# Optimization experiments

Measured on AMD Instinct MI355X. Metric: run time of the kernel, lower is better.

The kernel has to match this reference:

```python
import jax, jax.numpy as jnp
import numpy as np

B, H, W = 16, 1024, 1024
BOUNDARY_WEIGHT = 2.0
FOCAL_ALPHA = 0.25
FOCAL_GAMMA = 2.0
SMOOTH = 1e-6


def setup_inputs() -> dict:
    key = jax.random.key(0)
    k1, k2, k3 = jax.random.split(key, 3)
    pred_masks = jax.random.normal(k1, (B, 1, H, W), dtype=jnp.float32)
    gt_masks = jax.random.bernoulli(k2, 0.5, (B, 1, H, W)).astype(jnp.float32)
    pred_iou = jax.random.uniform(k3, (B, 1), dtype=jnp.float32)
    return {"pred_masks": pred_masks, "gt_masks": gt_masks, "pred_iou": pred_iou}


def _bce_with_logits(x, t):
    # stable: softplus(x) - x*t == -[t*log(sig(x)) + (1-t)*log(1-sig(x))]
    return jax.nn.softplus(x) - x * t


def reference(pred_masks, gt_masks, pred_iou):
    x, t = pred_masks, gt_masks
    ce = _bce_with_logits(x, t)                      # (B,1,H,W)
    p = jax.nn.sigmoid(x)

    # focal loss
    p_t = p * t + (1.0 - p) * (1.0 - t)
    alpha_t = FOCAL_ALPHA * t + (1.0 - FOCAL_ALPHA) * (1.0 - t)
    focal = jnp.mean(alpha_t * ce * (1.0 - p_t) ** FOCAL_GAMMA)

    # dice loss
    intersection = jnp.sum(p * t, axis=(2, 3))       # (B,1)
    union = jnp.sum(p, axis=(2, 3)) + jnp.sum(t, axis=(2, 3))
    dice = 1.0 - jnp.mean((2.0 * intersection + SMOOTH) / (union + SMOOTH))

    # boundary-weighted BCE. In the source, dist = EDT(mask) is 0 at every
    # background pixel and dist_inv = EDT(1-mask) is 0 at every foreground
    # pixel, so min(dist, dist_inv) == 0 <= 3 at EVERY pixel -> the weight
    # map is uniformly boundary_weight. Faithful equivalent:
    boundary = BOUNDARY_WEIGHT * jnp.mean(ce)

    total = focal + dice + 0.5 * boundary

    # IoU auxiliary loss (thresholded prediction; no grad flows through >0.5)
    pred_bin = (p > 0.5).astype(x.dtype)
    inter = jnp.sum(pred_bin * t, axis=(1, 2, 3))    # (B,)
    uni = jnp.sum(pred_bin, axis=(1, 2, 3)) + jnp.sum(t, axis=(1, 2, 3)) - inter
    actual_iou = (inter + SMOOTH) / (uni + SMOOTH)
    iou_loss = jnp.mean((jnp.squeeze(pred_iou) - actual_iou) ** 2)

    return total + 0.1 * iou_loss
```

## Files before the change

### kernel.cpp

```cpp
#include <hip/hip_runtime.h>
#include <math.h>


#define HW_PIX (1024 * 1024)
#define BATCH 16
constexpr int BPI = 256;
constexpr int GRID = BATCH * BPI;
constexpr int THREADS = 256;
constexpr int STRIDE_PX = BPI * THREADS * 4;
constexpr int ITERS = HW_PIX / STRIDE_PX;

__global__ __launch_bounds__(THREADS) void
loss_partial(const float* __restrict__ x, const float* __restrict__ t,
             float* __restrict__ acc) {
  const int b = blockIdx.x >> 8;
  const int chunk = blockIdx.x & (BPI - 1);
  const long base =
      (long)b * HW_PIX + ((long)chunk * THREADS + threadIdx.x) * 4;

  float fsum = 0.f, csum = 0.f, isum = 0.f, psum = 0.f;
  unsigned tcnt = 0, bicnt = 0, bpcnt = 0;

#pragma unroll
  for (int i = 0; i < ITERS; ++i) {
    const float4 xv = *(const float4*)(x + base + (long)i * STRIDE_PX);
    const float4 tv = *(const float4*)(t + base + (long)i * STRIDE_PX);
    const float* xs = reinterpret_cast<const float*>(&xv);
    const float* ts = reinterpret_cast<const float*>(&tv);
#pragma unroll
    for (int j = 0; j < 4; ++j) {
      const float xx = xs[j];
      const float tt = ts[j];
      const float e = __expf(-fabsf(xx));
      const float sp = 1.0f + e;
      const float r = __builtin_amdgcn_rcpf(sp);
      const float p = (xx >= 0.0f) ? r : e * r;
      const float ce = fmaxf(xx, 0.0f) - xx * tt + __logf(sp);
      const float om = fmaf(tt, 1.0f - 2.0f * p, p);
      const float at = 0.75f - 0.5f * tt;
      fsum += at * ce * om * om;
      csum += ce;
      isum = fmaf(p, tt, isum);
      psum += p;
      const unsigned long long mt = __ballot(tt != 0.0f);
      const unsigned long long mb = __ballot(xx > 0.0f);
      tcnt += (unsigned)__popcll(mt);
      bpcnt += (unsigned)__popcll(mb);
      bicnt += (unsigned)__popcll(mt & mb);
    }
  }

  __shared__ float red[THREADS / 64][7];
  const int lane = threadIdx.x & 63;
  const int wave = threadIdx.x >> 6;
  float vals[4] = {fsum, csum, isum, psum};
#pragma unroll
  for (int k = 0; k < 4; ++k) {
    float v = vals[k];
#pragma unroll
    for (int off = 32; off > 0; off >>= 1) v += __shfl_down(v, off);
    if (lane == 0) red[wave][k] = v;
  }
  if (lane == 0) {
    red[wave][4] = (float)tcnt;
    red[wave][5] = (float)bicnt;
    red[wave][6] = (float)bpcnt;
  }
  __syncthreads();
  if (threadIdx.x < 7) {
    acc[blockIdx.x * 7 + threadIdx.x] =
        red[0][threadIdx.x] + red[1][threadIdx.x] +
        red[2][threadIdx.x] + red[3][threadIdx.x];
  }
}

__global__ void loss_final(const float* __restrict__ acc,
                           const float* __restrict__ pred_iou,
                           float* __restrict__ out) {
  constexpr float SMOOTH = 1e-6f;
  __shared__ float fin[BATCH][7];
  const int tid = threadIdx.x;
  if (tid < BATCH * 7) {
    const int b = tid / 7, k = tid % 7;
    float s = 0.f;
    for (int i = 0; i < BPI; ++i)
      s += acc[(b * BPI + i) * 7 + k];
    fin[b][k] = s;
  }
  __syncthreads();
  if (tid < 64) {
    const int lane = tid;
    float F = 0.f, C = 0.f, D = 0.f, Q = 0.f;
    if (lane < BATCH) {
      F = fin[lane][0];
      C = fin[lane][1];
      const float I = fin[lane][2], P = fin[lane][3], T = fin[lane][4],
                  BI = fin[lane][5], BP = fin[lane][6];
      D = (2.0f * I + SMOOTH) / (P + T + SMOOTH);
      const float iou = (BI + SMOOTH) / (BP + T - BI + SMOOTH);
      const float d = pred_iou[lane] - iou;
      Q = d * d;
    }
#pragma unroll
    for (int off = 32; off > 0; off >>= 1) {
      F += __shfl_down(F, off);
      C += __shfl_down(C, off);
      D += __shfl_down(D, off);
      Q += __shfl_down(Q, off);
    }
    if (lane == 0) {
      const float invN = 1.0f / (float)((long)BATCH * HW_PIX);
      const float focal = F * invN;
      const float dice = 1.0f - D * (1.0f / (float)BATCH);
      const float half_boundary = C * invN;
      const float iou_loss = Q * (1.0f / (float)BATCH);
      out[0] = focal + dice + half_boundary + 0.1f * iou_loss;
    }
  }
}

extern "C" void kernel_launch(void* const* d_in, const int* in_sizes, int n_in,
                              void* d_out, int out_size, void* d_ws,
                              size_t ws_size, hipStream_t stream) {
  const float* x = (const float*)d_in[0];
  const float* t = (const float*)d_in[1];
  const float* piou = (const float*)d_in[2];
  float* acc = (float*)d_ws;

  loss_partial<<<GRID, THREADS, 0, stream>>>(x, t, acc);
  loss_final<<<1, 128, 0, stream>>>(acc, piou, (float*)d_out);
}
```

Before: 157.8 us.

## Issue all loads upfront via inline asm and consume with staged vmcnt waits

Halves the blocks per image so each thread handles eight float4 pairs. All sixteen global_load_dwordx4 instructions are issued up front through inline assembly using an SGPR base plus a VGPR offset. Each pair is then consumed after an explicit s_waitcnt vmcnt countdown. The intent is to keep many loads in flight per wave and to start compute as soon as the earliest data arrives, at the cost of more VGPRs and fewer blocks.

```diff
diff --git a/kernel.cpp b/kernel.cpp
--- a/kernel.cpp
+++ b/kernel.cpp
@@ -4,33 +4,42 @@
 
 #define HW_PIX (1024 * 1024)
 #define BATCH 16
-constexpr int BPI = 256;
+constexpr int BPI = 128;
 constexpr int GRID = BATCH * BPI;
 constexpr int THREADS = 256;
-constexpr int STRIDE_PX = BPI * THREADS * 4;
-constexpr int ITERS = HW_PIX / STRIDE_PX;
+constexpr unsigned SWEEP_B = BPI * THREADS * 16;
+
+typedef float vf4 __attribute__((ext_vector_type(4)));
 
 __global__ __launch_bounds__(THREADS) void
 loss_partial(const float* __restrict__ x, const float* __restrict__ t,
              float* __restrict__ acc) {
-  const int b = blockIdx.x >> 8;
+  const int b = blockIdx.x >> 7;
   const int chunk = blockIdx.x & (BPI - 1);
-  const long base =
-      (long)b * HW_PIX + ((long)chunk * THREADS + threadIdx.x) * 4;
+  const float* xb = x + (long)b * HW_PIX;
+  const float* tb = t + (long)b * HW_PIX;
+  const unsigned off0 = (chunk * THREADS + threadIdx.x) * 16u;
+
+  vf4 x0, x1, x2, x3, x4, x5, x6, x7;
+  vf4 t0, t1, t2, t3, t4, t5, t6, t7;
+
+#define ISSUE(i, xi, ti)                                              \
+  asm volatile("global_load_dwordx4 %0, %2, %3\n\t"                   \
+               "global_load_dwordx4 %1, %2, %4"                       \
+               : "=v"(xi), "=v"(ti)                                   \
+               : "v"(off0 + (unsigned)(i) * SWEEP_B), "s"(xb), "s"(tb));
+  ISSUE(0, x0, t0) ISSUE(1, x1, t1) ISSUE(2, x2, t2) ISSUE(3, x3, t3)
+  ISSUE(4, x4, t4) ISSUE(5, x5, t5) ISSUE(6, x6, t6) ISSUE(7, x7, t7)
+#undef ISSUE
 
   float fsum = 0.f, csum = 0.f, isum = 0.f, psum = 0.f;
   unsigned tcnt = 0, bicnt = 0, bpcnt = 0;
 
-#pragma unroll
-  for (int i = 0; i < ITERS; ++i) {
-    const float4 xv = *(const float4*)(x + base + (long)i * STRIDE_PX);
-    const float4 tv = *(const float4*)(t + base + (long)i * STRIDE_PX);
-    const float* xs = reinterpret_cast<const float*>(&xv);
-    const float* ts = reinterpret_cast<const float*>(&tv);
+  auto compute = [&](const vf4& xv, const vf4& tv) {
 #pragma unroll
     for (int j = 0; j < 4; ++j) {
-      const float xx = xs[j];
-      const float tt = ts[j];
+      const float xx = xv[j];
+      const float tt = tv[j];
       const float e = __expf(-fabsf(xx));
       const float sp = 1.0f + e;
       const float r = __builtin_amdgcn_rcpf(sp);
@@ -48,7 +57,20 @@
       bpcnt += (unsigned)__popcll(mb);
       bicnt += (unsigned)__popcll(mt & mb);
     }
-  }
+  };
+
+#define CONSUME(n, xi, ti)                                            \
+  asm volatile("s_waitcnt vmcnt(" #n ")" : "+v"(xi), "+v"(ti));       \
+  compute(xi, ti);
+  CONSUME(14, x0, t0)
+  CONSUME(12, x1, t1)
+  CONSUME(10, x2, t2)
+  CONSUME(8, x3, t3)
+  CONSUME(6, x4, t4)
+  CONSUME(4, x5, t5)
+  CONSUME(2, x6, t6)
+  CONSUME(0, x7, t7)
+#undef CONSUME
 
   __shared__ float red[THREADS / 64][7];
   const int lane = threadIdx.x & 63;
@@ -58,7 +80,7 @@
   for (int k = 0; k < 4; ++k) {
     float v = vals[k];
 #pragma unroll
-    for (int off = 32; off > 0; off >>= 1) v += __shfl_down(v, off);
+    for (int off2 = 32; off2 > 0; off2 >>= 1) v += __shfl_down(v, off2);
     if (lane == 0) red[wave][k] = v;
   }
   if (lane == 0) {
```

Result: faster. 150.9 us (-4.4%).
